# Kernel optimization log

Hardware: AMD Instinct MI355X
Metric: run time of the kernel (lower is better)

The kernel has to match this reference:

```python
import jax, jax.numpy as jnp
import numpy as np

SQRT2 = np.float32(np.sqrt(2.0))
D = 256


def setup_inputs() -> dict:
    key = jax.random.key(0)
    k1, = jax.random.split(key, 1)
    x = jax.random.normal(k1, (4, 1024, D), dtype=jnp.float32)
    weight = jnp.ones((D,), dtype=jnp.float32)
    bias = jnp.zeros((D,), dtype=jnp.float32)
    return {"x": x, "weight": weight, "bias": bias}


def reference(x, weight, bias):
    orig_shape = x.shape
    d = orig_shape[-1]
    flat = x.reshape(-1, d)  # [N, D]
    # Silverman 2d bandwidth: 0.9 * std(ddof=1, dim=-1) * D^(-1/5)
    bw = 0.9 * jnp.std(flat, axis=-1, ddof=1) * np.float32(d ** (-0.2))  # [N]
    # Pairwise Gaussian-kernel CDF, averaged over data points (dim 2).
    scaled = (flat[:, :, None] - flat[:, None, :]) / bw[:, None, None]  # [N, D, D]
    cdf = jnp.mean(0.5 * (1.0 + jax.lax.erf(scaled / SQRT2)), axis=2)  # [N, D]
    # Gaussian PPF (inverse CDF)
    normed = jax.lax.erf_inv(2.0 * cdf - 1.0) * SQRT2  # [N, D]
    out = normed.reshape(orig_shape) * weight + bias
    return out
```

## Files before the change

### kernel.cpp

```cpp
#include <hip/hip_runtime.h>
#include <math.h>

#define DD 256
#define NW 4

typedef float v2f __attribute__((ext_vector_type(2)));

template <int CTRL>
__device__ __forceinline__ float dpp_add(float x) {
    return x + __int_as_float(__builtin_amdgcn_update_dpp(
        0, __float_as_int(x), CTRL, 0xf, 0xf, false));
}
template <int CTRL>
__device__ __forceinline__ float dpp_mov_self(float x) {
    return __int_as_float(__builtin_amdgcn_update_dpp(
        __float_as_int(x), __float_as_int(x), CTRL, 0xf, 0xf, false));
}
__device__ __forceinline__ float wave_sum(float x) {
    x = dpp_add<0x111>(x); x = dpp_add<0x112>(x);
    x = dpp_add<0x114>(x); x = dpp_add<0x118>(x);
    x = dpp_add<0x142>(x); x = dpp_add<0x143>(x);
    return __int_as_float(__builtin_amdgcn_readlane(__float_as_int(x), 63));
}
__device__ __forceinline__ float wave_max(float x) {
    x = __builtin_fmaxf(x, dpp_mov_self<0x111>(x));
    x = __builtin_fmaxf(x, dpp_mov_self<0x112>(x));
    x = __builtin_fmaxf(x, dpp_mov_self<0x114>(x));
    x = __builtin_fmaxf(x, dpp_mov_self<0x118>(x));
    x = __builtin_fmaxf(x, dpp_mov_self<0x142>(x));
    x = __builtin_fmaxf(x, dpp_mov_self<0x143>(x));
    return __int_as_float(__builtin_amdgcn_readlane(__float_as_int(x), 63));
}
__device__ __forceinline__ float wave_min(float x) {
    x = __builtin_fminf(x, dpp_mov_self<0x111>(x));
    x = __builtin_fminf(x, dpp_mov_self<0x112>(x));
    x = __builtin_fminf(x, dpp_mov_self<0x114>(x));
    x = __builtin_fminf(x, dpp_mov_self<0x118>(x));
    x = __builtin_fminf(x, dpp_mov_self<0x142>(x));
    x = __builtin_fminf(x, dpp_mov_self<0x143>(x));
    return __int_as_float(__builtin_amdgcn_readlane(__float_as_int(x), 63));
}

__device__ __forceinline__ float ppf_from_y(float y) {
    float omy2 = __builtin_fmaf(-y, y, 1.0f);
    float wg = __builtin_fmaf(-__builtin_amdgcn_logf(omy2), 0.69314718056f, -2.5f);
    float p = 2.81022636e-08f;
    p = __builtin_fmaf(p, wg, 3.43273939e-07f);
    p = __builtin_fmaf(p, wg, -3.5233877e-06f);
    p = __builtin_fmaf(p, wg, -4.39150654e-06f);
    p = __builtin_fmaf(p, wg, 0.00021858087f);
    p = __builtin_fmaf(p, wg, -0.00125372503f);
    p = __builtin_fmaf(p, wg, -0.00417768164f);
    p = __builtin_fmaf(p, wg, 0.246640727f);
    p = __builtin_fmaf(p, wg, 1.50140941f);
    return p * y * 1.41421356237309505f;
}

__global__ __launch_bounds__(64 * NW, 4) void kd_layernorm_kernel(
        const float* __restrict__ x,
        const float* __restrict__ wgt,
        const float* __restrict__ bia,
        float* __restrict__ out) {
    const int lane = threadIdx.x & 63;
    const int wid  = threadIdx.x >> 6;
    const int row  = blockIdx.x * NW + wid;
    const float* xr = x + (size_t)row * DD;

    float u0 = xr[lane], u1 = xr[64 + lane], u2 = xr[128 + lane], u3 = xr[192 + lane];

    float ssum = wave_sum((u0 + u1) + (u2 + u3));
    float qsum = wave_sum(__builtin_fmaf(u0, u0, u1 * u1) +
                          __builtin_fmaf(u2, u2, u3 * u3));
    float xmax = wave_max(__builtin_fmaxf(__builtin_fmaxf(u0, u1),
                                          __builtin_fmaxf(u2, u3)));
    float xmin = wave_min(__builtin_fminf(__builtin_fminf(u0, u1),
                                          __builtin_fminf(u2, u3)));

    float var = (qsum - ssum * ssum * (1.0f / DD)) * (1.0f / (DD - 1));
    float bw = 0.9f * __builtin_sqrtf(var) * 0.32987697769322355f;
    float invbw = __builtin_amdgcn_rcpf(bw);
    float v0 = u0 * invbw, v1 = u1 * invbw, v2 = u2 * invbw, v3 = u3 * invbw;
    float meanv = ssum * invbw * (1.0f / DD);

    float L = (xmax - xmin) * invbw + 10.0f;
    float invL = __builtin_amdgcn_rcpf(L);
    int M = (int)__builtin_ceilf(0.70028175f * L);
    M = M < 1 ? 1 : (M > 96 ? 96 : M);
    M = __builtin_amdgcn_readfirstlane(M);

    v2f s1a = {__builtin_amdgcn_sinf(v0 * invL), __builtin_amdgcn_sinf(v1 * invL)};
    v2f s1b = {__builtin_amdgcn_sinf(v2 * invL), __builtin_amdgcn_sinf(v3 * invL)};
    v2f c1a = {__builtin_amdgcn_cosf(v0 * invL), __builtin_amdgcn_cosf(v1 * invL)};
    v2f c1b = {__builtin_amdgcn_cosf(v2 * invL), __builtin_amdgcn_cosf(v3 * invL)};

    v2f sma = s1a, smb = s1b, cma = c1a, cmb = c1b;
    v2f Ra = {0.f, 0.f}, Rb = {0.f, 0.f};

    float w1sq = 39.4784176044f * invL * invL;
    float g   = __builtin_amdgcn_exp2f(-0.72134752f * w1sq);
    float rr  = __builtin_amdgcn_exp2f(-2.16404256f * w1sq);
    const float rho = __builtin_amdgcn_exp2f(-1.44269504f * w1sq);
    float fm = 1.0f;

    #pragma clang loop unroll_count(1)
    for (int m = 1; m <= M; ++m) {
        v2f sp = sma + smb;
        v2f cp = cma + cmb;
        float Stot = wave_sum(sp.x + sp.y);
        float Ctot = wave_sum(cp.x + cp.y);
        float sc = g * 0.31830988618f * __builtin_amdgcn_rcpf(fm);
        float gC = Ctot * sc, gS = Stot * sc;
        v2f vgC = {gC, gC}, vgS = {gS, gS};
        Ra = __builtin_elementwise_fma(sma, vgC, Ra);
        Ra = __builtin_elementwise_fma(cma, -vgS, Ra);
        Rb = __builtin_elementwise_fma(smb, vgC, Rb);
        Rb = __builtin_elementwise_fma(cmb, -vgS, Rb);
        v2f nsa = __builtin_elementwise_fma(sma, c1a, cma * s1a);
        v2f nca = __builtin_elementwise_fma(cma, c1a, -(sma * s1a));
        v2f nsb = __builtin_elementwise_fma(smb, c1b, cmb * s1b);
        v2f ncb = __builtin_elementwise_fma(cmb, c1b, -(smb * s1b));
        sma = nsa; cma = nca; smb = nsb; cmb = ncb;
        g *= rr; rr *= rho; fm += 1.0f;
    }

    float vv[4] = {v0, v1, v2, v3};
    float Rv[4] = {Ra.x, Ra.y, Rb.x, Rb.y};
    #pragma unroll
    for (int a = 0; a < 4; ++a) {
        float y = 2.0f * __builtin_fmaf(vv[a] - meanv, invL, Rv[a] * (1.0f / DD));
        float normed = ppf_from_y(y);
        int idx = a * 64 + lane;
        out[(size_t)row * DD + idx] = __builtin_fmaf(normed, wgt[idx], bia[idx]);
    }
}

extern "C" void kernel_launch(void* const* d_in, const int* in_sizes, int n_in,
                              void* d_out, int out_size, void* d_ws, size_t ws_size,
                              hipStream_t stream) {
    const float* x = (const float*)d_in[0];
    const float* w = (const float*)d_in[1];
    const float* b = (const float*)d_in[2];
    float* out = (float*)d_out;
    const int nrows = in_sizes[0] / DD;
    kd_layernorm_kernel<<<nrows / NW, 64 * NW, 0, stream>>>(x, w, b, out);
}
```

Before: 67.56 us.

## Fix Fourier mode count and batch all wave reductions in unrolled passes

Replaces the data-dependent Fourier series loop (up to 96 modes, one serialized pair of wave reductions per mode) with a fixed 24-mode, fully unrolled three-phase scheme. The first pass computes per-lane partial sums for every mode, the second runs all reductions independently so the DPP chains can overlap, and the third rebuilds the per-element sum with a second sin/cos recurrence. Loads and stores become 16-byte vector accesses. The recurrence is computed twice and the PC/PS arrays raise register pressure. Capping at 24 modes may lose accuracy on rows whose range needs more modes.

After: 67.35 us. No clear change (-0.3%).

```diff
diff --git a/kernel.cpp b/kernel.cpp
--- a/kernel.cpp
+++ b/kernel.cpp
@@ -3,8 +3,10 @@
 
 #define DD 256
 #define NW 4
+#define MFIX 24
 
 typedef float v2f __attribute__((ext_vector_type(2)));
+typedef float v4f __attribute__((ext_vector_type(4)));
 
 template <int CTRL>
 __device__ __forceinline__ float dpp_add(float x) {
@@ -16,29 +18,32 @@
     return __int_as_float(__builtin_amdgcn_update_dpp(
         __float_as_int(x), __float_as_int(x), CTRL, 0xf, 0xf, false));
 }
-__device__ __forceinline__ float wave_sum(float x) {
+__device__ __forceinline__ float wave_sum_chain(float x) {
     x = dpp_add<0x111>(x); x = dpp_add<0x112>(x);
     x = dpp_add<0x114>(x); x = dpp_add<0x118>(x);
     x = dpp_add<0x142>(x); x = dpp_add<0x143>(x);
+    return x;
+}
+__device__ __forceinline__ float lane63(float x) {
     return __int_as_float(__builtin_amdgcn_readlane(__float_as_int(x), 63));
 }
-__device__ __forceinline__ float wave_max(float x) {
+__device__ __forceinline__ float wave_max_chain(float x) {
     x = __builtin_fmaxf(x, dpp_mov_self<0x111>(x));
     x = __builtin_fmaxf(x, dpp_mov_self<0x112>(x));
     x = __builtin_fmaxf(x, dpp_mov_self<0x114>(x));
     x = __builtin_fmaxf(x, dpp_mov_self<0x118>(x));
     x = __builtin_fmaxf(x, dpp_mov_self<0x142>(x));
     x = __builtin_fmaxf(x, dpp_mov_self<0x143>(x));
-    return __int_as_float(__builtin_amdgcn_readlane(__float_as_int(x), 63));
+    return x;
 }
-__device__ __forceinline__ float wave_min(float x) {
+__device__ __forceinline__ float wave_min_chain(float x) {
     x = __builtin_fminf(x, dpp_mov_self<0x111>(x));
     x = __builtin_fminf(x, dpp_mov_self<0x112>(x));
     x = __builtin_fminf(x, dpp_mov_self<0x114>(x));
     x = __builtin_fminf(x, dpp_mov_self<0x118>(x));
     x = __builtin_fminf(x, dpp_mov_self<0x142>(x));
     x = __builtin_fminf(x, dpp_mov_self<0x143>(x));
-    return __int_as_float(__builtin_amdgcn_readlane(__float_as_int(x), 63));
+    return x;
 }
 
 __device__ __forceinline__ float ppf_from_y(float y) {
@@ -64,74 +69,85 @@
     const int lane = threadIdx.x & 63;
     const int wid  = threadIdx.x >> 6;
     const int row  = blockIdx.x * NW + wid;
-    const float* xr = x + (size_t)row * DD;
 
-    float u0 = xr[lane], u1 = xr[64 + lane], u2 = xr[128 + lane], u3 = xr[192 + lane];
+    const v4f u = ((const v4f*)(x + (size_t)row * DD))[lane];
 
-    float ssum = wave_sum((u0 + u1) + (u2 + u3));
-    float qsum = wave_sum(__builtin_fmaf(u0, u0, u1 * u1) +
-                          __builtin_fmaf(u2, u2, u3 * u3));
-    float xmax = wave_max(__builtin_fmaxf(__builtin_fmaxf(u0, u1),
-                                          __builtin_fmaxf(u2, u3)));
-    float xmin = wave_min(__builtin_fminf(__builtin_fminf(u0, u1),
-                                          __builtin_fminf(u2, u3)));
+    float ssum = lane63(wave_sum_chain((u.x + u.y) + (u.z + u.w)));
+    float qsum = lane63(wave_sum_chain(__builtin_fmaf(u.x, u.x, u.y * u.y) +
+                                       __builtin_fmaf(u.z, u.z, u.w * u.w)));
+    float xmax = lane63(wave_max_chain(__builtin_fmaxf(__builtin_fmaxf(u.x, u.y),
+                                                       __builtin_fmaxf(u.z, u.w))));
+    float xmin = lane63(wave_min_chain(__builtin_fminf(__builtin_fminf(u.x, u.y),
+                                                       __builtin_fminf(u.z, u.w))));
 
     float var = (qsum - ssum * ssum * (1.0f / DD)) * (1.0f / (DD - 1));
     float bw = 0.9f * __builtin_sqrtf(var) * 0.32987697769322355f;
     float invbw = __builtin_amdgcn_rcpf(bw);
-    float v0 = u0 * invbw, v1 = u1 * invbw, v2 = u2 * invbw, v3 = u3 * invbw;
+    v4f v = u * invbw;
     float meanv = ssum * invbw * (1.0f / DD);
 
     float L = (xmax - xmin) * invbw + 10.0f;
     float invL = __builtin_amdgcn_rcpf(L);
-    int M = (int)__builtin_ceilf(0.70028175f * L);
-    M = M < 1 ? 1 : (M > 96 ? 96 : M);
-    M = __builtin_amdgcn_readfirstlane(M);
 
-    v2f s1a = {__builtin_amdgcn_sinf(v0 * invL), __builtin_amdgcn_sinf(v1 * invL)};
-    v2f s1b = {__builtin_amdgcn_sinf(v2 * invL), __builtin_amdgcn_sinf(v3 * invL)};
-    v2f c1a = {__builtin_amdgcn_cosf(v0 * invL), __builtin_amdgcn_cosf(v1 * invL)};
-    v2f c1b = {__builtin_amdgcn_cosf(v2 * invL), __builtin_amdgcn_cosf(v3 * invL)};
+    v4f ph = v * invL;
+    v4f s1, c1;
+    s1.x = __builtin_amdgcn_sinf(ph.x); s1.y = __builtin_amdgcn_sinf(ph.y);
+    s1.z = __builtin_amdgcn_sinf(ph.z); s1.w = __builtin_amdgcn_sinf(ph.w);
+    c1.x = __builtin_amdgcn_cosf(ph.x); c1.y = __builtin_amdgcn_cosf(ph.y);
+    c1.z = __builtin_amdgcn_cosf(ph.z); c1.w = __builtin_amdgcn_cosf(ph.w);
 
-    v2f sma = s1a, smb = s1b, cma = c1a, cmb = c1b;
-    v2f Ra = {0.f, 0.f}, Rb = {0.f, 0.f};
-
-    float w1sq = 39.4784176044f * invL * invL;
-    float g   = __builtin_amdgcn_exp2f(-0.72134752f * w1sq);
-    float rr  = __builtin_amdgcn_exp2f(-2.16404256f * w1sq);
-    const float rho = __builtin_amdgcn_exp2f(-1.44269504f * w1sq);
-    float fm = 1.0f;
-
-    #pragma clang loop unroll_count(1)
-    for (int m = 1; m <= M; ++m) {
-        v2f sp = sma + smb;
-        v2f cp = cma + cmb;
-        float Stot = wave_sum(sp.x + sp.y);
-        float Ctot = wave_sum(cp.x + cp.y);
-        float sc = g * 0.31830988618f * __builtin_amdgcn_rcpf(fm);
-        float gC = Ctot * sc, gS = Stot * sc;
-        v2f vgC = {gC, gC}, vgS = {gS, gS};
-        Ra = __builtin_elementwise_fma(sma, vgC, Ra);
-        Ra = __builtin_elementwise_fma(cma, -vgS, Ra);
-        Rb = __builtin_elementwise_fma(smb, vgC, Rb);
-        Rb = __builtin_elementwise_fma(cmb, -vgS, Rb);
-        v2f nsa = __builtin_elementwise_fma(sma, c1a, cma * s1a);
-        v2f nca = __builtin_elementwise_fma(cma, c1a, -(sma * s1a));
-        v2f nsb = __builtin_elementwise_fma(smb, c1b, cmb * s1b);
-        v2f ncb = __builtin_elementwise_fma(cmb, c1b, -(smb * s1b));
-        sma = nsa; cma = nca; smb = nsb; cmb = ncb;
-        g *= rr; rr *= rho; fm += 1.0f;
+    float PC[MFIX], PS[MFIX];
+    {
+        v4f sm = s1, cm = c1;
+        #pragma unroll
+        for (int m = 0; m < MFIX; ++m) {
+            PS[m] = (sm.x + sm.y) + (sm.z + sm.w);
+            PC[m] = (cm.x + cm.y) + (cm.z + cm.w);
+            v4f ns = __builtin_elementwise_fma(sm, c1, cm * s1);
+            v4f nc = __builtin_elementwise_fma(cm, c1, -(sm * s1));
+            sm = ns; cm = nc;
+        }
     }
 
-    float vv[4] = {v0, v1, v2, v3};
-    float Rv[4] = {Ra.x, Ra.y, Rb.x, Rb.y};
-    #pragma unroll
-    for (int a = 0; a < 4; ++a) {
-        float y = 2.0f * __builtin_fmaf(vv[a] - meanv, invL, Rv[a] * (1.0f / DD));
-        float normed = ppf_from_y(y);
-        int idx = a * 64 + lane;
-        out[(size_t)row * DD + idx] = __builtin_fmaf(normed, wgt[idx], bia[idx]);
+    {
+        float w1sq = 39.4784176044f * invL * invL;
+        float g   = __builtin_amdgcn_exp2f(-0.72134752f * w1sq);
+        float rr  = __builtin_amdgcn_exp2f(-2.16404256f * w1sq);
+        const float rho = __builtin_amdgcn_exp2f(-1.44269504f * w1sq);
+        #pragma unroll
+        for (int m = 0; m < MFIX; ++m) {
+            float Ct = lane63(wave_sum_chain(PC[m]));
+            float St = lane63(wave_sum_chain(PS[m]));
+            float sc = g * (0.31830988618f / (float)(m + 1));
+            PC[m] = Ct * sc;
+            PS[m] = St * sc;
+            g *= rr; rr *= rho;
+        }
     }
+
+    v4f R = {0.f, 0.f, 0.f, 0.f};
+    {
+        v4f sm = s1, cm = c1;
+        #pragma unroll
+        for (int m = 0; m < MFIX; ++m) {
+            v4f vgC = {PC[m], PC[m], PC[m], PC[m]};
+            v4f vgS = {PS[m], PS[m], PS[m], PS[m]};
+            R = __builtin_elementwise_fma(sm, vgC, R);
+            R = __builtin_elementwise_fma(cm, -vgS, R);
+            v4f ns = __builtin_elementwise_fma(sm, c1, cm * s1);
+            v4f nc = __builtin_elementwise_fma(cm, c1, -(sm * s1));
+            sm = ns; cm = nc;
+        }
+    }
+
+    const v4f wv = ((const v4f*)wgt)[lane];
+    const v4f bv = ((const v4f*)bia)[lane];
+    v4f o;
+    o.x = __builtin_fmaf(ppf_from_y(2.0f * __builtin_fmaf(v.x - meanv, invL, R.x * (1.0f / DD))), wv.x, bv.x);
+    o.y = __builtin_fmaf(ppf_from_y(2.0f * __builtin_fmaf(v.y - meanv, invL, R.y * (1.0f / DD))), wv.y, bv.y);
+    o.z = __builtin_fmaf(ppf_from_y(2.0f * __builtin_fmaf(v.z - meanv, invL, R.z * (1.0f / DD))), wv.z, bv.z);
+    o.w = __builtin_fmaf(ppf_from_y(2.0f * __builtin_fmaf(v.w - meanv, invL, R.w * (1.0f / DD))), wv.w, bv.w);
+    ((v4f*)(out + (size_t)row * DD))[lane] = o;
 }
 
 extern "C" void kernel_launch(void* const* d_in, const int* in_sizes, int n_in,
```
